# Kernel tuning notes

Hardware: AMD Instinct MI355X
Metric: run time of the kernel (lower is better)

Reference implementation:

```python
import jax, jax.numpy as jnp
import numpy as np

NUM_NODES = 200000
NUM_EDGES = 600000
NUM_GRAPHS = 10000
BN_EPS = 1e-5


def setup_inputs() -> dict:
    key = jax.random.key(0)
    ks = jax.random.split(key, 10)
    x = jax.random.normal(ks[0], (NUM_NODES, 78), dtype=jnp.float32)
    edge_index = jax.random.randint(ks[1], (2, NUM_EDGES), 0, NUM_NODES, dtype=jnp.int64 if jax.config.jax_enable_x64 else jnp.int32)
    batch = jnp.sort(jax.random.randint(ks[2], (NUM_NODES,), 0, NUM_GRAPHS))
    def glorot(k, shape):
        fan_in, fan_out = shape[-2], shape[-1]
        s = jnp.sqrt(2.0 / (fan_in + fan_out))
        return jax.random.normal(k, shape, dtype=jnp.float32) * s
    return {
        "x": x,
        "edge_index": edge_index,
        "batch": batch,
        "W1_0": glorot(ks[3], (78, 128)),
        "b1_0": jnp.zeros((128,), jnp.float32),
        "W2_0": glorot(ks[4], (128, 128)),
        "b2_0": jnp.zeros((128,), jnp.float32),
        "g_0": jnp.ones((128,), jnp.float32),
        "be_0": jnp.zeros((128,), jnp.float32),
        "W1s": glorot(ks[5], (4, 128, 128)),
        "b1s": jnp.zeros((4, 128), jnp.float32),
        "W2s": glorot(ks[6], (4, 128, 128)),
        "b2s": jnp.zeros((4, 128), jnp.float32),
        "gs": jnp.ones((4, 128), jnp.float32),
        "bes": jnp.zeros((4, 128), jnp.float32),
        "fcW": glorot(ks[7], (128, 64)),
        "fcb": jnp.zeros((64,), jnp.float32),
    }


def _batchnorm(h, gamma, beta):
    # BatchNorm1d with batch statistics (training-mode normalization)
    mean = h.mean(axis=0)
    var = h.var(axis=0)  # biased, as torch uses for normalization
    return gamma * (h - mean) * jax.lax.rsqrt(var + BN_EPS) + beta


def _gin_block(h, src, dst, W1, b1, W2, b2, gamma, beta):
    # GINConv (eps=0): MLP(x + sum of neighbor messages), then ReLU + BN
    agg = jax.ops.segment_sum(h[src], dst, num_segments=NUM_NODES)  # [N, d]
    z = h + agg
    z = jax.nn.relu(z @ W1 + b1) @ W2 + b2
    z = jax.nn.relu(z)
    return _batchnorm(z, gamma, beta)


def reference(x, edge_index, batch, W1_0, b1_0, W2_0, b2_0, g_0, be_0,
              W1s, b1s, W2s, b2s, gs, bes, fcW, fcb):
    src, dst = edge_index[0], edge_index[1]
    h = _gin_block(x, src, dst, W1_0, b1_0, W2_0, b2_0, g_0, be_0)  # [N, 128]

    def body(h, params):
        W1, b1, W2, b2, g, be = params
        return _gin_block(h, src, dst, W1, b1, W2, b2, g, be), None

    h, _ = jax.lax.scan(body, h, (W1s, b1s, W2s, b2s, gs, bes))

    pooled = jax.ops.segment_sum(h, batch, num_segments=NUM_GRAPHS)  # [G, 128]
    out = jax.nn.relu(pooled @ fcW + fcb)  # [G, 64]; dropout is identity at eval
    return out
```

## Files before the change

kernel.cpp:

```cpp
#include <hip/hip_runtime.h>
#include <hip/hip_bf16.h>

#define NN 200000
#define NE 600000
#define NG 10000
#define NCH 98
#define NTILE 3125

typedef __attribute__((ext_vector_type(8))) short bfrag;
typedef __attribute__((ext_vector_type(4))) float f32x4;
typedef unsigned short u16;

static __device__ __forceinline__ u16 f2b(float x) {
  __hip_bfloat16 b = __float2bfloat16(x);
  return __builtin_bit_cast(u16, b);
}
static __device__ __forceinline__ float b2f(u16 u) {
  __hip_bfloat16 b = __builtin_bit_cast(__hip_bfloat16, u);
  return __bfloat162float(b);
}
static __device__ __forceinline__ void split(float v, u16& hi, u16& lo) {
  hi = f2b(v);
  lo = f2b(v - b2f(hi));
}

__global__ void prep_kernel(const float* __restrict__ W1_0, const float* __restrict__ W2_0,
                            const float* __restrict__ W1s, const float* __restrict__ W2s,
                            u16* __restrict__ wf) {
  int i = blockIdx.x * 256 + threadIdx.x;
  if (i >= 312 * 64) return;
  int t = i >> 6, lane = i & 63;
  const float* W;
  int KS, ct, kk, Krows, base, half;
  if (t < 24) {
    W = W1_0; KS = 3; ct = t / 3; kk = t - ct * 3; Krows = 78; base = 0; half = 12288;
  } else if (t < 56) {
    int u = t - 24;
    W = W2_0; KS = 4; ct = u >> 2; kk = u & 3; Krows = 128; base = 24576; half = 16384;
  } else {
    int u = t - 56;
    int j = u >> 6, r = u & 63;
    KS = 4; Krows = 128; half = 16384;
    if (r < 32) {
      W = W1s + j * 16384; ct = r >> 2; kk = r & 3; base = 57344 + j * 65536;
    } else {
      W = W2s + j * 16384; r -= 32; ct = r >> 2; kk = r & 3; base = 57344 + j * 65536 + 32768;
    }
  }
  int col = ct * 16 + (lane & 15);
  int idx = ((ct * KS + kk) * 64 + lane) * 8;
  for (int jj = 0; jj < 8; jj++) {
    int k = kk * 32 + 8 * (lane >> 4) + jj;
    float v = (k < Krows) ? W[k * 128 + col] : 0.f;
    u16 hi, lo;
    split(v, hi, lo);
    wf[base + idx + jj] = hi;
    wf[base + half + idx + jj] = lo;
  }
}

__global__ void hist_kernel(const int* __restrict__ dst, int* __restrict__ deg) {
  int e = blockIdx.x * 256 + threadIdx.x;
  if (e < NE) atomicAdd(&deg[dst[e]], 1);
}

__global__ void scan1_kernel(const int* __restrict__ deg, int* __restrict__ csum) {
  __shared__ int s[256];
  int base = blockIdx.x * 2048 + threadIdx.x * 8;
  int t = 0;
#pragma unroll
  for (int j = 0; j < 8; j++) {
    int idx = base + j;
    if (idx < NN) t += deg[idx];
  }
  s[threadIdx.x] = t;
  __syncthreads();
  for (int o = 128; o > 0; o >>= 1) {
    if (threadIdx.x < o) s[threadIdx.x] += s[threadIdx.x + o];
    __syncthreads();
  }
  if (threadIdx.x == 0) csum[blockIdx.x] = s[0];
}

__global__ void scan2_kernel(int* __restrict__ csum, int* __restrict__ rowptr) {
  int acc = 0;
  for (int i = 0; i < NCH; i++) {
    int v = csum[i];
    csum[i] = acc;
    acc += v;
  }
  rowptr[NN] = acc;
}

__global__ void scan3_kernel(const int* deg, const int* __restrict__ csum,
                             int* __restrict__ rowptr, int* cursor) {
  __shared__ int s[256];
  int tid = threadIdx.x;
  int base = blockIdx.x * 2048 + tid * 8;
  int loc[8];
  int t = 0;
#pragma unroll
  for (int j = 0; j < 8; j++) {
    int idx = base + j;
    int d = (idx < NN) ? deg[idx] : 0;
    loc[j] = t;
    t += d;
  }
  s[tid] = t;
  __syncthreads();
  for (int o = 1; o < 256; o <<= 1) {
    int u = (tid >= o) ? s[tid - o] : 0;
    __syncthreads();
    s[tid] += u;
    __syncthreads();
  }
  int off = csum[blockIdx.x] + s[tid] - t;
#pragma unroll
  for (int j = 0; j < 8; j++) {
    int idx = base + j;
    if (idx < NN) {
      int r = off + loc[j];
      rowptr[idx] = r;
      cursor[idx] = r;
    }
  }
}

__global__ void scatter_kernel(const int* __restrict__ src, const int* __restrict__ dst,
                               int* __restrict__ cursor, int* __restrict__ csr_src) {
  int e = blockIdx.x * 256 + threadIdx.x;
  if (e < NE) {
    int p = atomicAdd(&cursor[dst[e]], 1);
    csr_src[p] = src[e];
  }
}

template <bool FIRST>
__global__ __launch_bounds__(512, 4) void fused_kernel(
    const float* __restrict__ xin, const u16* __restrict__ hin,
    const float* __restrict__ ss,
    const int* __restrict__ rowptr, const int* __restrict__ csr_src,
    const u16* __restrict__ w1hi, const u16* __restrict__ w1lo,
    const u16* __restrict__ w2hi, const u16* __restrict__ w2lo,
    const float* __restrict__ b1, const float* __restrict__ b2,
    u16* __restrict__ hout, float* __restrict__ stats) {
  constexpr int KS1 = FIRST ? 3 : 4;
  constexpr int AH = 0, AL = 8704, TH = 17408, TL = 26112;
  __shared__ u16 lds[34816];
  const int tid = threadIdx.x;
  const int w = tid >> 6, l = tid & 63;
  const int l15 = l & 15, lg = l >> 4;
  const float bb1 = b1[w * 16 + l15];
  const float bb2 = b2[w * 16 + l15];
  float s_acc = 0.f, q_acc = 0.f;

  if (FIRST) {
    const float2* x2 = reinterpret_cast<const float2*>(xin);
    for (int tile = blockIdx.x; tile < NTILE; tile += gridDim.x) {
      const int rows0 = tile * 64;
      for (int j = 0; j < 8; j++) {
        int row = w * 8 + j;
        int node = rows0 + row;
        int beg = rowptr[node], end = rowptr[node + 1];
        int f0 = l * 2;
        if (f0 < 78) {
          size_t fv = (size_t)(f0 >> 1);
          float2 acc = x2[(size_t)node * 39 + fv];
          for (int i = beg; i < end; i += 4) {
            int last = end - 1;
            int i1 = min(i + 1, last), i2 = min(i + 2, last), i3 = min(i + 3, last);
            int s0 = csr_src[i], s1 = csr_src[i1], s2 = csr_src[i2], s3 = csr_src[i3];
            float2 v0 = x2[(size_t)s0 * 39 + fv];
            float2 v1 = x2[(size_t)s1 * 39 + fv];
            float2 v2 = x2[(size_t)s2 * 39 + fv];
            float2 v3 = x2[(size_t)s3 * 39 + fv];
            int rem = end - i;
            float m1 = rem > 1 ? 1.f : 0.f, m2 = rem > 2 ? 1.f : 0.f, m3 = rem > 3 ? 1.f : 0.f;
            acc.x += v0.x + m1 * v1.x + m2 * v2.x + m3 * v3.x;
            acc.y += v0.y + m1 * v1.y + m2 * v2.y + m3 * v3.y;
          }
          ushort2 oh, ol;
          split(acc.x, oh.x, ol.x);
          split(acc.y, oh.y, ol.y);
          *reinterpret_cast<ushort2*>(&lds[AH + row * 136 + f0]) = oh;
          *reinterpret_cast<ushort2*>(&lds[AL + row * 136 + f0]) = ol;
        } else if (f0 < 96) {
          ushort2 z = {0, 0};
          *reinterpret_cast<ushort2*>(&lds[AH + row * 136 + f0]) = z;
          *reinterpret_cast<ushort2*>(&lds[AL + row * 136 + f0]) = z;
        }
      }
      bfrag w1h[KS1], w1l[KS1];
#pragma unroll
      for (int kk = 0; kk < KS1; kk++) {
        int fi = ((w * KS1 + kk) * 64 + l) * 8;
        w1h[kk] = *reinterpret_cast<const bfrag*>(&w1hi[fi]);
        w1l[kk] = *reinterpret_cast<const bfrag*>(&w1lo[fi]);
      }
      __syncthreads();
#pragma unroll
      for (int rt = 0; rt < 4; rt++) {
        f32x4 acc = {bb1, bb1, bb1, bb1};
        const int arow = (rt * 16 + l15) * 136 + 8 * lg;
#pragma unroll
        for (int kk = 0; kk < KS1; kk++) {
          bfrag ah = *reinterpret_cast<const bfrag*>(&lds[AH + arow + kk * 32]);
          bfrag al = *reinterpret_cast<const bfrag*>(&lds[AL + arow + kk * 32]);
          acc = __builtin_amdgcn_mfma_f32_16x16x32_bf16(al, w1h[kk], acc, 0, 0, 0);
          acc = __builtin_amdgcn_mfma_f32_16x16x32_bf16(ah, w1l[kk], acc, 0, 0, 0);
          acc = __builtin_amdgcn_mfma_f32_16x16x32_bf16(ah, w1h[kk], acc, 0, 0, 0);
        }
#pragma unroll
        for (int r = 0; r < 4; r++) {
          float v = fmaxf(acc[r], 0.f);
          u16 hi, lo;
          split(v, hi, lo);
          int off = (rt * 16 + 4 * lg + r) * 136 + w * 16 + l15;
          lds[TH + off] = hi;
          lds[TL + off] = lo;
        }
      }
      bfrag w2h[4], w2l[4];
#pragma unroll
      for (int kk = 0; kk < 4; kk++) {
        int fi = ((w * 4 + kk) * 64 + l) * 8;
        w2h[kk] = *reinterpret_cast<const bfrag*>(&w2hi[fi]);
        w2l[kk] = *reinterpret_cast<const bfrag*>(&w2lo[fi]);
      }
      __syncthreads();
      u16 o16[16];
#pragma unroll
      for (int rt = 0; rt < 4; rt++) {
        f32x4 acc = {bb2, bb2, bb2, bb2};
        const int arow = (rt * 16 + l15) * 136 + 8 * lg;
#pragma unroll
        for (int kk = 0; kk < 4; kk++) {
          bfrag th = *reinterpret_cast<const bfrag*>(&lds[TH + arow + kk * 32]);
          bfrag tl = *reinterpret_cast<const bfrag*>(&lds[TL + arow + kk * 32]);
          acc = __builtin_amdgcn_mfma_f32_16x16x32_bf16(tl, w2h[kk], acc, 0, 0, 0);
          acc = __builtin_amdgcn_mfma_f32_16x16x32_bf16(th, w2l[kk], acc, 0, 0, 0);
          acc = __builtin_amdgcn_mfma_f32_16x16x32_bf16(th, w2h[kk], acc, 0, 0, 0);
        }
#pragma unroll
        for (int r = 0; r < 4; r++) {
          float v = fmaxf(acc[r], 0.f);
          s_acc += v;
          q_acc += v * v;
          o16[rt * 4 + r] = f2b(v);
        }
      }
      __syncthreads();
#pragma unroll
      for (int rt = 0; rt < 4; rt++)
#pragma unroll
        for (int r = 0; r < 4; r++)
          lds[TH + (rt * 16 + 4 * lg + r) * 136 + w * 16 + l15] = o16[rt * 4 + r];
      __syncthreads();
#pragma unroll
      for (int p2 = 0; p2 < 2; p2++) {
        int row = p2 * 32 + (tid >> 4);
        int c8 = tid & 15;
        bfrag vv = *reinterpret_cast<const bfrag*>(&lds[TH + row * 136 + c8 * 8]);
        *reinterpret_cast<bfrag*>(&hout[(size_t)(rows0 + row) * 128 + c8 * 8]) = vv;
      }
      __syncthreads();
    }
  } else {
    const bfrag* hp = reinterpret_cast<const bfrag*>(hin);
    const int k8v = l15;
    const int k8 = l15 * 8;
    float sc8[8], sh8[8];
#pragma unroll
    for (int j = 0; j < 8; j++) {
      sc8[j] = ss[k8 + j];
      sh8[j] = ss[128 + k8 + j];
    }

    int tile0 = blockIdx.x;
#pragma unroll
    for (int p = 0; p < 2; p++) {
      int row = w * 8 + p * 4 + lg;
      int node = tile0 * 64 + row;
      int beg = rowptr[node], end = rowptr[node + 1];
      float a[8];
      bfrag vs = hp[(size_t)node * 16 + k8v];
#pragma unroll
      for (int j = 0; j < 8; j++) a[j] = b2f((u16)vs[j]);
      for (int i = beg; i < end; i += 4) {
        int last = end - 1;
        int i1 = min(i + 1, last), i2 = min(i + 2, last), i3 = min(i + 3, last);
        int s0 = csr_src[i], s1 = csr_src[i1], s2 = csr_src[i2], s3 = csr_src[i3];
        bfrag v0 = hp[(size_t)s0 * 16 + k8v];
        bfrag v1 = hp[(size_t)s1 * 16 + k8v];
        bfrag v2 = hp[(size_t)s2 * 16 + k8v];
        bfrag v3 = hp[(size_t)s3 * 16 + k8v];
        int rem = end - i;
        float m1 = rem > 1 ? 1.f : 0.f, m2 = rem > 2 ? 1.f : 0.f, m3 = rem > 3 ? 1.f : 0.f;
#pragma unroll
        for (int j = 0; j < 8; j++)
          a[j] += (b2f((u16)v0[j]) + m1 * b2f((u16)v1[j])) +
                  (m2 * b2f((u16)v2[j]) + m3 * b2f((u16)v3[j]));
      }
      float cnt = (float)(end - beg + 1);
      bfrag oh, ol;
#pragma unroll
      for (int j = 0; j < 8; j++) {
        float t = a[j] * sc8[j] + cnt * sh8[j];
        u16 hi, lo;
        split(t, hi, lo);
        oh[j] = (short)hi;
        ol[j] = (short)lo;
      }
      *reinterpret_cast<bfrag*>(&lds[AH + row * 136 + k8]) = oh;
      *reinterpret_cast<bfrag*>(&lds[AL + row * 136 + k8]) = ol;
    }
    __syncthreads();

    for (int tile = tile0; tile < NTILE; tile += gridDim.x) {
      const int rows0 = tile * 64;
      int tn = tile + gridDim.x;
      bool np = tn < NTILE;
      int tnc = np ? tn : tile;

      int begN[2], endN[2];
#pragma unroll
      for (int p = 0; p < 2; p++) {
        int nodeN = tnc * 64 + w * 8 + p * 4 + lg;
        begN[p] = rowptr[nodeN];
        endN[p] = rowptr[nodeN + 1];
      }

      bfrag w1h[4], w1l[4];
#pragma unroll
      for (int kk = 0; kk < 4; kk++) {
        int fi = ((w * 4 + kk) * 64 + l) * 8;
        w1h[kk] = *reinterpret_cast<const bfrag*>(&w1hi[fi]);
        w1l[kk] = *reinterpret_cast<const bfrag*>(&w1lo[fi]);
      }
      f32x4 t1[4];
#pragma unroll
      for (int rt = 0; rt < 4; rt++) {
        f32x4 acc = {bb1, bb1, bb1, bb1};
        const int arow = (rt * 16 + l15) * 136 + 8 * lg;
#pragma unroll
        for (int kk = 0; kk < 4; kk++) {
          bfrag ah = *reinterpret_cast<const bfrag*>(&lds[AH + arow + kk * 32]);
          bfrag al = *reinterpret_cast<const bfrag*>(&lds[AL + arow + kk * 32]);
          acc = __builtin_amdgcn_mfma_f32_16x16x32_bf16(al, w1h[kk], acc, 0, 0, 0);
          acc = __builtin_amdgcn_mfma_f32_16x16x32_bf16(ah, w1l[kk], acc, 0, 0, 0);
          acc = __builtin_amdgcn_mfma_f32_16x16x32_bf16(ah, w1h[kk], acc, 0, 0, 0);
        }
        t1[rt] = acc;
      }
      __syncthreads();

      int s0[2], s1[2], s2[2], s3[2];
      float m0[2], m1[2], m2[2], m3[2], cntN[2];
#pragma unroll
      for (int p = 0; p < 2; p++) {
        int beg = begN[p], end = endN[p];
        int deg = end - beg;
        int last = end - 1;
        int i0 = beg, i1 = min(beg + 1, last), i2 = min(beg + 2, last), i3 = min(beg + 3, last);
        if (deg <= 0) { i0 = 0; i1 = 0; i2 = 0; i3 = 0; }
        s0[p] = csr_src[i0];
        s1[p] = csr_src[i1];
        s2[p] = csr_src[i2];
        s3[p] = csr_src[i3];
        m0[p] = deg > 0 ? 1.f : 0.f;
        m1[p] = deg > 1 ? 1.f : 0.f;
        m2[p] = deg > 2 ? 1.f : 0.f;
        m3[p] = deg > 3 ? 1.f : 0.f;
        cntN[p] = (float)(deg + 1);
      }

#pragma unroll
      for (int rt = 0; rt < 4; rt++) {
#pragma unroll
        for (int r = 0; r < 4; r++) {
          float v = fmaxf(t1[rt][r], 0.f);
          u16 hi, lo;
          split(v, hi, lo);
          int off = (rt * 16 + 4 * lg + r) * 136 + w * 16 + l15;
          lds[TH + off] = hi;
          lds[TL + off] = lo;
        }
      }
      bfrag w2h[4], w2l[4];
#pragma unroll
      for (int kk = 0; kk < 4; kk++) {
        int fi = ((w * 4 + kk) * 64 + l) * 8;
        w2h[kk] = *reinterpret_cast<const bfrag*>(&w2hi[fi]);
        w2l[kk] = *reinterpret_cast<const bfrag*>(&w2lo[fi]);
      }
      __syncthreads();

      bfrag selfN[2], nb0[2], nb1[2], nb2[2], nb3[2];
#pragma unroll
      for (int p = 0; p < 2; p++) {
        int nodeN = tnc * 64 + w * 8 + p * 4 + lg;
        selfN[p] = hp[(size_t)nodeN * 16 + k8v];
        nb0[p] = hp[(size_t)s0[p] * 16 + k8v];
        nb1[p] = hp[(size_t)s1[p] * 16 + k8v];
        nb2[p] = hp[(size_t)s2[p] * 16 + k8v];
        nb3[p] = hp[(size_t)s3[p] * 16 + k8v];
      }

      u16 o16[16];
#pragma unroll
      for (int rt = 0; rt < 4; rt++) {
        f32x4 acc = {bb2, bb2, bb2, bb2};
        const int arow = (rt * 16 + l15) * 136 + 8 * lg;
#pragma unroll
        for (int kk = 0; kk < 4; kk++) {
          bfrag th = *reinterpret_cast<const bfrag*>(&lds[TH + arow + kk * 32]);
          bfrag tl = *reinterpret_cast<const bfrag*>(&lds[TL + arow + kk * 32]);
          acc = __builtin_amdgcn_mfma_f32_16x16x32_bf16(tl, w2h[kk], acc, 0, 0, 0);
          acc = __builtin_amdgcn_mfma_f32_16x16x32_bf16(th, w2l[kk], acc, 0, 0, 0);
          acc = __builtin_amdgcn_mfma_f32_16x16x32_bf16(th, w2h[kk], acc, 0, 0, 0);
        }
#pragma unroll
        for (int r = 0; r < 4; r++) {
          float v = fmaxf(acc[r], 0.f);
          s_acc += v;
          q_acc += v * v;
          o16[rt * 4 + r] = f2b(v);
        }
      }
      __syncthreads();

      if (np) {
#pragma unroll
        for (int p = 0; p < 2; p++) {
          int row = w * 8 + p * 4 + lg;
          float a[8];
#pragma unroll
          for (int j = 0; j < 8; j++) a[j] = b2f((u16)selfN[p][j]);
#pragma unroll
          for (int j = 0; j < 8; j++)
            a[j] += (m0[p] * b2f((u16)nb0[p][j]) + m1[p] * b2f((u16)nb1[p][j])) +
                    (m2[p] * b2f((u16)nb2[p][j]) + m3[p] * b2f((u16)nb3[p][j]));
          int beg = begN[p], end = endN[p];
          for (int i = beg + 4; i < end; i += 4) {
            int last = end - 1;
            int i1 = min(i + 1, last), i2 = min(i + 2, last), i3 = min(i + 3, last);
            int t0 = csr_src[i], t1i = csr_src[i1], t2 = csr_src[i2], t3 = csr_src[i3];
            bfrag v0 = hp[(size_t)t0 * 16 + k8v];
            bfrag v1 = hp[(size_t)t1i * 16 + k8v];
            bfrag v2 = hp[(size_t)t2 * 16 + k8v];
            bfrag v3 = hp[(size_t)t3 * 16 + k8v];
            int rem = end - i;
            float n1 = rem > 1 ? 1.f : 0.f, n2 = rem > 2 ? 1.f : 0.f, n3 = rem > 3 ? 1.f : 0.f;
#pragma unroll
            for (int j = 0; j < 8; j++)
              a[j] += (b2f((u16)v0[j]) + n1 * b2f((u16)v1[j])) +
                      (n2 * b2f((u16)v2[j]) + n3 * b2f((u16)v3[j]));
          }
          bfrag oh, ol;
#pragma unroll
          for (int j = 0; j < 8; j++) {
            float t = a[j] * sc8[j] + cntN[p] * sh8[j];
            u16 hi, lo;
            split(t, hi, lo);
            oh[j] = (short)hi;
            ol[j] = (short)lo;
          }
          *reinterpret_cast<bfrag*>(&lds[AH + row * 136 + k8]) = oh;
          *reinterpret_cast<bfrag*>(&lds[AL + row * 136 + k8]) = ol;
        }
      }

#pragma unroll
      for (int rt = 0; rt < 4; rt++)
#pragma unroll
        for (int r = 0; r < 4; r++)
          lds[TH + (rt * 16 + 4 * lg + r) * 136 + w * 16 + l15] = o16[rt * 4 + r];
      __syncthreads();

#pragma unroll
      for (int p2 = 0; p2 < 2; p2++) {
        int row = p2 * 32 + (tid >> 4);
        int c8 = tid & 15;
        bfrag vv = *reinterpret_cast<const bfrag*>(&lds[TH + row * 136 + c8 * 8]);
        *reinterpret_cast<bfrag*>(&hout[(size_t)(rows0 + row) * 128 + c8 * 8]) = vv;
      }
    }
  }
  s_acc += __shfl_xor(s_acc, 16);
  s_acc += __shfl_xor(s_acc, 32);
  q_acc += __shfl_xor(q_acc, 16);
  q_acc += __shfl_xor(q_acc, 32);
  if (lg == 0) {
    atomicAdd(&stats[w * 16 + l15], s_acc);
    atomicAdd(&stats[128 + w * 16 + l15], q_acc);
  }
}

__global__ void bn_kernel(const float* __restrict__ stats, const float* __restrict__ gamma,
                          const float* __restrict__ beta, float* __restrict__ ss) {
  int c = threadIdx.x;
  float mean = stats[c] * (1.f / NN);
  float var = stats[128 + c] * (1.f / NN) - mean * mean;
  var = fmaxf(var, 0.f);
  float sc = gamma[c] * rsqrtf(var + 1e-5f);
  ss[c] = sc;
  ss[128 + c] = beta[c] - mean * sc;
}

__global__ void pool_kernel(const u16* __restrict__ h, const float* __restrict__ ss,
                            const int* __restrict__ batch, float* __restrict__ pooled) {
  int c = threadIdx.x;
  int n0 = blockIdx.x * 128;
  int n1 = min(n0 + 128, NN);
  float sc = ss[c], sh = ss[128 + c];
  float acc = 0.f;
  float cnt = 0.f;
  int gprev = batch[n0];
  for (int n = n0; n < n1; n++) {
    int g = batch[n];
    if (g != gprev) {
      atomicAdd(&pooled[gprev * 128 + c], sc * acc + cnt * sh);
      acc = 0.f;
      cnt = 0.f;
      gprev = g;
    }
    acc += b2f(h[(size_t)n * 128 + c]);
    cnt += 1.f;
  }
  atomicAdd(&pooled[gprev * 128 + c], sc * acc + cnt * sh);
}

__global__ void fc_kernel(const float* __restrict__ pooled, const float* __restrict__ fcW,
                          const float* __restrict__ fcb, float* __restrict__ out) {
  int i = blockIdx.x * 256 + threadIdx.x;
  if (i >= NG * 64) return;
  int g = i >> 6, o = i & 63;
  float acc = fcb[o];
#pragma unroll 8
  for (int k = 0; k < 128; k++) acc += pooled[g * 128 + k] * fcW[k * 64 + o];
  out[i] = fmaxf(acc, 0.f);
}

extern "C" void kernel_launch(void* const* d_in, const int* in_sizes, int n_in,
                              void* d_out, int out_size, void* d_ws, size_t ws_size,
                              hipStream_t stream) {
  const float* x = (const float*)d_in[0];
  const int* ei = (const int*)d_in[1];
  const int* src = ei;
  const int* dst = ei + NE;
  const int* batch = (const int*)d_in[2];
  const float* W1_0 = (const float*)d_in[3];
  const float* b1_0 = (const float*)d_in[4];
  const float* W2_0 = (const float*)d_in[5];
  const float* b2_0 = (const float*)d_in[6];
  const float* g_0 = (const float*)d_in[7];
  const float* be_0 = (const float*)d_in[8];
  const float* W1s = (const float*)d_in[9];
  const float* b1s = (const float*)d_in[10];
  const float* W2s = (const float*)d_in[11];
  const float* b2s = (const float*)d_in[12];
  const float* gs = (const float*)d_in[13];
  const float* bes = (const float*)d_in[14];
  const float* fcW = (const float*)d_in[15];
  const float* fcb = (const float*)d_in[16];

  char* ws = (char*)d_ws;
  u16* buf0 = (u16*)(ws + 0);
  u16* buf1 = (u16*)(ws + 51200000);
  float* POOLED = (float*)(ws + 102400000);
  float* STATS = (float*)(ws + 107520000);
  float* SS = (float*)(ws + 107521024);
  u16* WF = (u16*)(ws + 107522048);
  int* ROWPTR = (int*)(ws + 108161024);
  int* CURSOR = (int*)(ws + 108961040);
  int* CSRC = (int*)(ws + 109761040);
  int* CSUM = (int*)(ws + 112161040);

  prep_kernel<<<78, 256, 0, stream>>>(W1_0, W2_0, W1s, W2s, WF);

  hipMemsetAsync(CURSOR, 0, NN * 4, stream);
  hist_kernel<<<(NE + 255) / 256, 256, 0, stream>>>(dst, CURSOR);
  scan1_kernel<<<NCH, 256, 0, stream>>>(CURSOR, CSUM);
  scan2_kernel<<<1, 1, 0, stream>>>(CSUM, ROWPTR);
  scan3_kernel<<<NCH, 256, 0, stream>>>(CURSOR, CSUM, ROWPTR, CURSOR);
  scatter_kernel<<<(NE + 255) / 256, 256, 0, stream>>>(src, dst, CURSOR, CSRC);

  u16* buf[2] = {buf0, buf1};
  hipMemsetAsync(STATS, 0, 1024, stream);
  fused_kernel<true><<<512, 512, 0, stream>>>(x, nullptr, nullptr, ROWPTR, CSRC,
                                              WF, WF + 12288, WF + 24576, WF + 40960,
                                              b1_0, b2_0, buf0, STATS);
  bn_kernel<<<1, 128, 0, stream>>>(STATS, g_0, be_0, SS);

  for (int L = 1; L < 5; L++) {
    int j = L - 1;
    const u16* hin = buf[(L + 1) & 1];
    u16* hb = buf[L & 1];
    hipMemsetAsync(STATS, 0, 1024, stream);
    const u16* wl = WF + 57344 + j * 65536;
    fused_kernel<false><<<512, 512, 0, stream>>>(nullptr, hin, SS, ROWPTR, CSRC,
                                                 wl, wl + 16384, wl + 32768, wl + 49152,
                                                 b1s + j * 128, b2s + j * 128, hb, STATS);
    bn_kernel<<<1, 128, 0, stream>>>(STATS, gs + j * 128, bes + j * 128, SS);
  }

  hipMemsetAsync(POOLED, 0, (size_t)NG * 128 * 4, stream);
  pool_kernel<<<(NN + 127) / 128, 128, 0, stream>>>(buf[0], SS, batch, POOLED);
  fc_kernel<<<(NG * 64 + 255) / 256, 256, 0, stream>>>(POOLED, fcW, fcb, (float*)d_out);
}
```

Measured before the change: 740.2 us.

## Process two tiles per iteration with batched gathers instead of cross-tile prefetch

```diff
diff --git a/kernel.cpp b/kernel.cpp
--- a/kernel.cpp
+++ b/kernel.cpp
@@ -145,7 +145,6 @@
     const float* __restrict__ b1, const float* __restrict__ b2,
     u16* __restrict__ hout, float* __restrict__ stats) {
   constexpr int KS1 = FIRST ? 3 : 4;
-  constexpr int AH = 0, AL = 8704, TH = 17408, TL = 26112;
   __shared__ u16 lds[34816];
   const int tid = threadIdx.x;
   const int w = tid >> 6, l = tid & 63;
@@ -155,6 +154,7 @@
   float s_acc = 0.f, q_acc = 0.f;
 
   if (FIRST) {
+    constexpr int AH = 0, AL = 8704, TH = 17408, TL = 26112;
     const float2* x2 = reinterpret_cast<const float2*>(xin);
     for (int tile = blockIdx.x; tile < NTILE; tile += gridDim.x) {
       const int rows0 = tile * 64;
@@ -276,58 +276,74 @@
       sh8[j] = ss[128 + k8 + j];
     }
 
-    int tile0 = blockIdx.x;
-#pragma unroll
-    for (int p = 0; p < 2; p++) {
-      int row = w * 8 + p * 4 + lg;
-      int node = tile0 * 64 + row;
-      int beg = rowptr[node], end = rowptr[node + 1];
-      float a[8];
-      bfrag vs = hp[(size_t)node * 16 + k8v];
-#pragma unroll
-      for (int j = 0; j < 8; j++) a[j] = b2f((u16)vs[j]);
-      for (int i = beg; i < end; i += 4) {
+    for (int t0 = blockIdx.x * 2; t0 < NTILE; t0 += gridDim.x * 2) {
+      const bool has1 = (t0 + 1) < NTILE;
+
+      int begA[4], endA[4];
+      bfrag selfA[4], nb0A[4], nb1A[4], nb2A[4], nb3A[4];
+#pragma unroll
+      for (int pp = 0; pp < 4; pp++) {
+        int ti = (pp >= 2 && !has1) ? t0 : t0 + (pp >> 1);
+        int row = w * 8 + (pp & 1) * 4 + lg;
+        int node = ti * 64 + row;
+        int beg = rowptr[node], end = rowptr[node + 1];
+        int deg = end - beg;
         int last = end - 1;
-        int i1 = min(i + 1, last), i2 = min(i + 2, last), i3 = min(i + 3, last);
-        int s0 = csr_src[i], s1 = csr_src[i1], s2 = csr_src[i2], s3 = csr_src[i3];
-        bfrag v0 = hp[(size_t)s0 * 16 + k8v];
-        bfrag v1 = hp[(size_t)s1 * 16 + k8v];
-        bfrag v2 = hp[(size_t)s2 * 16 + k8v];
-        bfrag v3 = hp[(size_t)s3 * 16 + k8v];
-        int rem = end - i;
-        float m1 = rem > 1 ? 1.f : 0.f, m2 = rem > 2 ? 1.f : 0.f, m3 = rem > 3 ? 1.f : 0.f;
+        int i0 = beg, i1 = min(beg + 1, last), i2 = min(beg + 2, last), i3 = min(beg + 3, last);
+        if (deg <= 0) { i0 = 0; i1 = 0; i2 = 0; i3 = 0; }
+        int s0 = csr_src[i0], s1 = csr_src[i1], s2 = csr_src[i2], s3 = csr_src[i3];
+        begA[pp] = beg;
+        endA[pp] = end;
+        selfA[pp] = hp[(size_t)node * 16 + k8v];
+        nb0A[pp] = hp[(size_t)s0 * 16 + k8v];
+        nb1A[pp] = hp[(size_t)s1 * 16 + k8v];
+        nb2A[pp] = hp[(size_t)s2 * 16 + k8v];
+        nb3A[pp] = hp[(size_t)s3 * 16 + k8v];
+      }
+
+#pragma unroll
+      for (int pp = 0; pp < 4; pp++) {
+        if (pp >= 2 && !has1) continue;
+        int row = w * 8 + (pp & 1) * 4 + lg;
+        int rb = (pp >> 1) * 17408;
+        int beg = begA[pp], end = endA[pp];
+        int deg = end - beg;
+        float m0 = deg > 0 ? 1.f : 0.f, m1 = deg > 1 ? 1.f : 0.f;
+        float m2 = deg > 2 ? 1.f : 0.f, m3 = deg > 3 ? 1.f : 0.f;
+        float a[8];
+#pragma unroll
+        for (int j = 0; j < 8; j++) a[j] = b2f((u16)selfA[pp][j]);
 #pragma unroll
         for (int j = 0; j < 8; j++)
-          a[j] += (b2f((u16)v0[j]) + m1 * b2f((u16)v1[j])) +
-                  (m2 * b2f((u16)v2[j]) + m3 * b2f((u16)v3[j]));
-      }
-      float cnt = (float)(end - beg + 1);
-      bfrag oh, ol;
-#pragma unroll
-      for (int j = 0; j < 8; j++) {
-        float t = a[j] * sc8[j] + cnt * sh8[j];
-        u16 hi, lo;
-        split(t, hi, lo);
-        oh[j] = (short)hi;
-        ol[j] = (short)lo;
-      }
-      *reinterpret_cast<bfrag*>(&lds[AH + row * 136 + k8]) = oh;
-      *reinterpret_cast<bfrag*>(&lds[AL + row * 136 + k8]) = ol;
-    }
-    __syncthreads();
-
-    for (int tile = tile0; tile < NTILE; tile += gridDim.x) {
-      const int rows0 = tile * 64;
-      int tn = tile + gridDim.x;
-      bool np = tn < NTILE;
-      int tnc = np ? tn : tile;
-
-      int begN[2], endN[2];
-#pragma unroll
-      for (int p = 0; p < 2; p++) {
-        int nodeN = tnc * 64 + w * 8 + p * 4 + lg;
-        begN[p] = rowptr[nodeN];
-        endN[p] = rowptr[nodeN + 1];
+          a[j] += (m0 * b2f((u16)nb0A[pp][j]) + m1 * b2f((u16)nb1A[pp][j])) +
+                  (m2 * b2f((u16)nb2A[pp][j]) + m3 * b2f((u16)nb3A[pp][j]));
+        for (int i = beg + 4; i < end; i += 4) {
+          int last = end - 1;
+          int i1 = min(i + 1, last), i2 = min(i + 2, last), i3 = min(i + 3, last);
+          int t0i = csr_src[i], t1i = csr_src[i1], t2i = csr_src[i2], t3i = csr_src[i3];
+          bfrag v0 = hp[(size_t)t0i * 16 + k8v];
+          bfrag v1 = hp[(size_t)t1i * 16 + k8v];
+          bfrag v2 = hp[(size_t)t2i * 16 + k8v];
+          bfrag v3 = hp[(size_t)t3i * 16 + k8v];
+          int rem = end - i;
+          float n1 = rem > 1 ? 1.f : 0.f, n2 = rem > 2 ? 1.f : 0.f, n3 = rem > 3 ? 1.f : 0.f;
+#pragma unroll
+          for (int j = 0; j < 8; j++)
+            a[j] += (b2f((u16)v0[j]) + n1 * b2f((u16)v1[j])) +
+                    (n2 * b2f((u16)v2[j]) + n3 * b2f((u16)v3[j]));
+        }
+        float cnt = (float)(deg + 1);
+        bfrag oh, ol;
+#pragma unroll
+        for (int j = 0; j < 8; j++) {
+          float t = a[j] * sc8[j] + cnt * sh8[j];
+          u16 hi, lo;
+          split(t, hi, lo);
+          oh[j] = (short)hi;
+          ol[j] = (short)lo;
+        }
+        *reinterpret_cast<bfrag*>(&lds[rb + row * 136 + k8]) = oh;
+        *reinterpret_cast<bfrag*>(&lds[rb + 8704 + row * 136 + k8]) = ol;
       }
 
       bfrag w1h[4], w1l[4];
@@ -337,53 +353,65 @@
         w1h[kk] = *reinterpret_cast<const bfrag*>(&w1hi[fi]);
         w1l[kk] = *reinterpret_cast<const bfrag*>(&w1lo[fi]);
       }
-      f32x4 t1[4];
+      __syncthreads();
+
+      f32x4 acc0[4], acc1[4];
 #pragma unroll
       for (int rt = 0; rt < 4; rt++) {
         f32x4 acc = {bb1, bb1, bb1, bb1};
         const int arow = (rt * 16 + l15) * 136 + 8 * lg;
 #pragma unroll
         for (int kk = 0; kk < 4; kk++) {
-          bfrag ah = *reinterpret_cast<const bfrag*>(&lds[AH + arow + kk * 32]);
-          bfrag al = *reinterpret_cast<const bfrag*>(&lds[AL + arow + kk * 32]);
+          bfrag ah = *reinterpret_cast<const bfrag*>(&lds[arow + kk * 32]);
+          bfrag al = *reinterpret_cast<const bfrag*>(&lds[8704 + arow + kk * 32]);
           acc = __builtin_amdgcn_mfma_f32_16x16x32_bf16(al, w1h[kk], acc, 0, 0, 0);
           acc = __builtin_amdgcn_mfma_f32_16x16x32_bf16(ah, w1l[kk], acc, 0, 0, 0);
           acc = __builtin_amdgcn_mfma_f32_16x16x32_bf16(ah, w1h[kk], acc, 0, 0, 0);
         }
-        t1[rt] = acc;
-      }
-      __syncthreads();
-
-      int s0[2], s1[2], s2[2], s3[2];
-      float m0[2], m1[2], m2[2], m3[2], cntN[2];
-#pragma unroll
-      for (int p = 0; p < 2; p++) {
-        int beg = begN[p], end = endN[p];
-        int deg = end - beg;
-        int last = end - 1;
-        int i0 = beg, i1 = min(beg + 1, last), i2 = min(beg + 2, last), i3 = min(beg + 3, last);
-        if (deg <= 0) { i0 = 0; i1 = 0; i2 = 0; i3 = 0; }
-        s0[p] = csr_src[i0];
-        s1[p] = csr_src[i1];
-        s2[p] = csr_src[i2];
-        s3[p] = csr_src[i3];
-        m0[p] = deg > 0 ? 1.f : 0.f;
-        m1[p] = deg > 1 ? 1.f : 0.f;
-        m2[p] = deg > 2 ? 1.f : 0.f;
-        m3[p] = deg > 3 ? 1.f : 0.f;
-        cntN[p] = (float)(deg + 1);
-      }
+        acc0[rt] = acc;
+      }
+      if (has1) {
+#pragma unroll
+        for (int rt = 0; rt < 4; rt++) {
+          f32x4 acc = {bb1, bb1, bb1, bb1};
+          const int arow = (rt * 16 + l15) * 136 + 8 * lg;
+#pragma unroll
+          for (int kk = 0; kk < 4; kk++) {
+            bfrag ah = *reinterpret_cast<const bfrag*>(&lds[17408 + arow + kk * 32]);
+            bfrag al = *reinterpret_cast<const bfrag*>(&lds[26112 + arow + kk * 32]);
+            acc = __builtin_amdgcn_mfma_f32_16x16x32_bf16(al, w1h[kk], acc, 0, 0, 0);
+            acc = __builtin_amdgcn_mfma_f32_16x16x32_bf16(ah, w1l[kk], acc, 0, 0, 0);
+            acc = __builtin_amdgcn_mfma_f32_16x16x32_bf16(ah, w1h[kk], acc, 0, 0, 0);
+          }
+          acc1[rt] = acc;
+        }
+      }
+      __syncthreads();
 
 #pragma unroll
       for (int rt = 0; rt < 4; rt++) {
 #pragma unroll
         for (int r = 0; r < 4; r++) {
-          float v = fmaxf(t1[rt][r], 0.f);
+          float v = fmaxf(acc0[rt][r], 0.f);
           u16 hi, lo;
           split(v, hi, lo);
           int off = (rt * 16 + 4 * lg + r) * 136 + w * 16 + l15;
-          lds[TH + off] = hi;
-          lds[TL + off] = lo;
+          lds[off] = hi;
+          lds[8704 + off] = lo;
+        }
+      }
+      if (has1) {
+#pragma unroll
+        for (int rt = 0; rt < 4; rt++) {
+#pragma unroll
+          for (int r = 0; r < 4; r++) {
+            float v = fmaxf(acc1[rt][r], 0.f);
+            u16 hi, lo;
+            split(v, hi, lo);
+            int off = (rt * 16 + 4 * lg + r) * 136 + w * 16 + l15;
+            lds[17408 + off] = hi;
+            lds[26112 + off] = lo;
+          }
         }
       }
       bfrag w2h[4], w2l[4];
@@ -395,26 +423,15 @@
       }
       __syncthreads();
 
-      bfrag selfN[2], nb0[2], nb1[2], nb2[2], nb3[2];
-#pragma unroll
-      for (int p = 0; p < 2; p++) {
-        int nodeN = tnc * 64 + w * 8 + p * 4 + lg;
-        selfN[p] = hp[(size_t)nodeN * 16 + k8v];
-        nb0[p] = hp[(size_t)s0[p] * 16 + k8v];
-        nb1[p] = hp[(size_t)s1[p] * 16 + k8v];
-        nb2[p] = hp[(size_t)s2[p] * 16 + k8v];
-        nb3[p] = hp[(size_t)s3[p] * 16 + k8v];
-      }
-
-      u16 o16[16];
+      u16 o0[16], o1[16];
 #pragma unroll
       for (int rt = 0; rt < 4; rt++) {
         f32x4 acc = {bb2, bb2, bb2, bb2};
         const int arow = (rt * 16 + l15) * 136 + 8 * lg;
 #pragma unroll
         for (int kk = 0; kk < 4; kk++) {
-          bfrag th = *reinterpret_cast<const bfrag*>(&lds[TH + arow + kk * 32]);
-          bfrag tl = *reinterpret_cast<const bfrag*>(&lds[TL + arow + kk * 32]);
+          bfrag th = *reinterpret_cast<const bfrag*>(&lds[arow + kk * 32]);
+          bfrag tl = *reinterpret_cast<const bfrag*>(&lds[8704 + arow + kk * 32]);
           acc = __builtin_amdgcn_mfma_f32_16x16x32_bf16(tl, w2h[kk], acc, 0, 0, 0);
           acc = __builtin_amdgcn_mfma_f32_16x16x32_bf16(th, w2l[kk], acc, 0, 0, 0);
           acc = __builtin_amdgcn_mfma_f32_16x16x32_bf16(th, w2h[kk], acc, 0, 0, 0);
@@ -424,66 +441,64 @@
           float v = fmaxf(acc[r], 0.f);
           s_acc += v;
           q_acc += v * v;
-          o16[rt * 4 + r] = f2b(v);
-        }
-      }
-      __syncthreads();
-
-      if (np) {
-#pragma unroll
-        for (int p = 0; p < 2; p++) {
-          int row = w * 8 + p * 4 + lg;
-          float a[8];
-#pragma unroll
-          for (int j = 0; j < 8; j++) a[j] = b2f((u16)selfN[p][j]);
-#pragma unroll
-          for (int j = 0; j < 8; j++)
-            a[j] += (m0[p] * b2f((u16)nb0[p][j]) + m1[p] * b2f((u16)nb1[p][j])) +
-                    (m2[p] * b2f((u16)nb2[p][j]) + m3[p] * b2f((u16)nb3[p][j]));
-          int beg = begN[p], end = endN[p];
-          for (int i = beg + 4; i < end; i += 4) {
-            int last = end - 1;
-            int i1 = min(i + 1, last), i2 = min(i + 2, last), i3 = min(i + 3, last);
-            int t0 = csr_src[i], t1i = csr_src[i1], t2 = csr_src[i2], t3 = csr_src[i3];
-            bfrag v0 = hp[(size_t)t0 * 16 + k8v];
-            bfrag v1 = hp[(size_t)t1i * 16 + k8v];
-            bfrag v2 = hp[(size_t)t2 * 16 + k8v];
-            bfrag v3 = hp[(size_t)t3 * 16 + k8v];
-            int rem = end - i;
-            float n1 = rem > 1 ? 1.f : 0.f, n2 = rem > 2 ? 1.f : 0.f, n3 = rem > 3 ? 1.f : 0.f;
-#pragma unroll
-            for (int j = 0; j < 8; j++)
-              a[j] += (b2f((u16)v0[j]) + n1 * b2f((u16)v1[j])) +
-                      (n2 * b2f((u16)v2[j]) + n3 * b2f((u16)v3[j]));
+          o0[rt * 4 + r] = f2b(v);
+        }
+      }
+      if (has1) {
+#pragma unroll
+        for (int rt = 0; rt < 4; rt++) {
+          f32x4 acc = {bb2, bb2, bb2, bb2};
+          const int arow = (rt * 16 + l15) * 136 + 8 * lg;
+#pragma unroll
+          for (int kk = 0; kk < 4; kk++) {
+            bfrag th = *reinterpret_cast<const bfrag*>(&lds[17408 + arow + kk * 32]);
+            bfrag tl = *reinterpret_cast<const bfrag*>(&lds[26112 + arow + kk * 32]);
+            acc = __builtin_amdgcn_mfma_f32_16x16x32_bf16(tl, w2h[kk], acc, 0, 0, 0);
+            acc = __builtin_amdgcn_mfma_f32_16x16x32_bf16(th, w2l[kk], acc, 0, 0, 0);
+            acc = __builtin_amdgcn_mfma_f32_16x16x32_bf16(th, w2h[kk], acc, 0, 0, 0);
           }
-          bfrag oh, ol;
-#pragma unroll
-          for (int j = 0; j < 8; j++) {
-            float t = a[j] * sc8[j] + cntN[p] * sh8[j];
-            u16 hi, lo;
-            split(t, hi, lo);
-            oh[j] = (short)hi;
-            ol[j] = (short)lo;
+#pragma unroll
+          for (int r = 0; r < 4; r++) {
+            float v = fmaxf(acc[r], 0.f);
+            s_acc += v;
+            q_acc += v * v;
+            o1[rt * 4 + r] = f2b(v);
           }
-          *reinterpret_cast<bfrag*>(&lds[AH + row * 136 + k8]) = oh;
-          *reinterpret_cast<bfrag*>(&lds[AL + row * 136 + k8]) = ol;
-        }
-      }
+        }
+      }
+      __syncthreads();
 
 #pragma unroll
       for (int rt = 0; rt < 4; rt++)
 #pragma unroll
         for (int r = 0; r < 4; r++)
-          lds[TH + (rt * 16 + 4 * lg + r) * 136 + w * 16 + l15] = o16[rt * 4 + r];
+          lds[(rt * 16 + 4 * lg + r) * 136 + w * 16 + l15] = o0[rt * 4 + r];
+      if (has1) {
+#pragma unroll
+        for (int rt = 0; rt < 4; rt++)
+#pragma unroll
+          for (int r = 0; r < 4; r++)
+            lds[17408 + (rt * 16 + 4 * lg + r) * 136 + w * 16 + l15] = o1[rt * 4 + r];
+      }
       __syncthreads();
 
 #pragma unroll
       for (int p2 = 0; p2 < 2; p2++) {
         int row = p2 * 32 + (tid >> 4);
         int c8 = tid & 15;
-        bfrag vv = *reinterpret_cast<const bfrag*>(&lds[TH + row * 136 + c8 * 8]);
-        *reinterpret_cast<bfrag*>(&hout[(size_t)(rows0 + row) * 128 + c8 * 8]) = vv;
-      }
+        bfrag vv = *reinterpret_cast<const bfrag*>(&lds[row * 136 + c8 * 8]);
+        *reinterpret_cast<bfrag*>(&hout[(size_t)(t0 * 64 + row) * 128 + c8 * 8]) = vv;
+      }
+      if (has1) {
+#pragma unroll
+        for (int p2 = 0; p2 < 2; p2++) {
+          int row = p2 * 32 + (tid >> 4);
+          int c8 = tid & 15;
+          bfrag vv = *reinterpret_cast<const bfrag*>(&lds[17408 + row * 136 + c8 * 8]);
+          *reinterpret_cast<bfrag*>(&hout[(size_t)((t0 + 1) * 64 + row) * 128 + c8 * 8]) = vv;
+        }
+      }
+      __syncthreads();
     }
   }
   s_acc += __shfl_xor(s_acc, 16);
```

Measured after the change: 1.131 ms. 52.8% more time.
